# Performance work log

Hardware: AMD Instinct MI355X
Metric: run time of the kernel (lower is better)

## Reference

```python
import jax, jax.numpy as jnp
import numpy as np

T, B, H, I = 128, 32, 256, 256


def setup_inputs() -> dict:
    key = jax.random.key(0)
    ks = jax.random.split(key, 8)
    s = 0.05
    embs = jax.random.normal(ks[0], (T, B, I), jnp.float32)
    lens = jax.random.randint(ks[1], (B,), 1, T + 1)  # lengths in [1, T]
    W_ih = jax.random.normal(ks[2], (4 * H, I), jnp.float32) * s
    W_hh = jax.random.normal(ks[3], (4 * H, H), jnp.float32) * s
    b_ih = jax.random.normal(ks[4], (4 * H,), jnp.float32) * s
    b_hh = jax.random.normal(ks[5], (4 * H,), jnp.float32) * s
    W_a = jax.random.normal(ks[6], (H, 2 * H), jnp.float32) * s  # attention combine (Luong-style)
    b_a = jax.random.normal(ks[7], (H,), jnp.float32) * s
    return {"embs": embs, "lens": lens, "W_ih": W_ih, "W_hh": W_hh,
            "b_ih": b_ih, "b_hh": b_hh, "W_a": W_a, "b_a": b_a}


def reference(embs, lens, W_ih, W_hh, b_ih, b_hh, W_a, b_a):
    Tn, Bn, _ = embs.shape
    Hn = W_hh.shape[1]
    t_idx = jnp.arange(Tn)

    def step(carry, inp):
        h, c, buf, h_fin, c_fin = carry  # h,c: [B,H]; buf: [T,B,H] history of outputs
        t, emb = inp
        # dot-product attention of current hidden over past outputs (steps < t)
        scores = jnp.einsum('tbh,bh->tb', buf, h)
        valid = (t_idx < t)[:, None]
        alpha = jax.nn.softmax(jnp.where(valid, scores, -1e9), axis=0)
        ctx = jnp.einsum('tb,tbh->bh', alpha, buf)
        h_att = jnp.tanh(jnp.concatenate([ctx, h], axis=-1) @ W_a.T + b_a)
        h = jnp.where(t > 0, h_att, h)  # no history at t=0
        # standard PyTorch LSTM cell (gate order i,f,g,o)
        gates = emb @ W_ih.T + b_ih + h @ W_hh.T + b_hh
        i_g, f_g, g_g, o_g = jnp.split(gates, 4, axis=-1)
        c = jax.nn.sigmoid(f_g) * c + jax.nn.sigmoid(i_g) * jnp.tanh(g_g)
        h = jax.nn.sigmoid(o_g) * jnp.tanh(c)
        buf = buf.at[t].set(h)
        take = (t == lens - 1)[:, None]
        h_fin = jnp.where(take, h, h_fin)
        c_fin = jnp.where(take, c, c_fin)
        return (h, c, buf, h_fin, c_fin), h

    z = jnp.zeros((Bn, Hn), embs.dtype)
    buf0 = jnp.zeros((Tn, Bn, Hn), embs.dtype)
    carry, output = jax.lax.scan(step, (z, z, buf0, z, z), (t_idx, embs))
    # output: [T,B,H]; final (h,c) gathered at t == lens-1: [B,H]
    return output, carry[3], carry[4]
```

## Files before the change

### kernel.cpp

```cpp
#include <hip/hip_runtime.h>


#define T_DIM 128
#define B_DIM 32

typedef _Float16 half2_t __attribute__((ext_vector_type(2)));

static __device__ __forceinline__ unsigned pack2(float a, float b) {
  half2_t h;
  h.x = (_Float16)a;
  h.y = (_Float16)b;
  return __builtin_bit_cast(unsigned, h);
}

static __device__ __forceinline__ float dot2f(unsigned w, unsigned v, float acc) {
  half2_t a = __builtin_bit_cast(half2_t, w);
  half2_t b = __builtin_bit_cast(half2_t, v);
#if __has_builtin(__builtin_amdgcn_fdot2)
  return __builtin_amdgcn_fdot2(a, b, acc, false);
#else
  return acc + (float)a.x * (float)b.x + (float)a.y * (float)b.y;
#endif
}

static __device__ __forceinline__ float dot8(uint4 w, uint4 v, float acc) {
  acc = dot2f(w.x, v.x, acc);
  acc = dot2f(w.y, v.y, acc);
  acc = dot2f(w.z, v.z, acc);
  acc = dot2f(w.w, v.w, acc);
  return acc;
}

static __device__ __forceinline__ float lo16(unsigned u) {
  return (float)__builtin_bit_cast(half2_t, u).x;
}
static __device__ __forceinline__ float hi16(unsigned u) {
  return (float)__builtin_bit_cast(half2_t, u).y;
}

static __device__ __forceinline__ float fsig(float x) {
  return __builtin_amdgcn_rcpf(1.f + __expf(-x));
}
static __device__ __forceinline__ float ftanh(float x) {
  float e = __expf(2.f * x);
  return 1.f - 2.f * __builtin_amdgcn_rcpf(e + 1.f);
}

__global__ void pack_weights(const float* __restrict__ W_ih, const float* __restrict__ W_hh,
                             const float* __restrict__ W_a, float* __restrict__ W_ihT,
                             uint4* __restrict__ Whh_pack, uint4* __restrict__ Wa_pack,
                             unsigned long long* __restrict__ ywp,
                             unsigned long long* __restrict__ psx) {
  int n = blockIdx.x * 256 + threadIdx.x;
  {
    int k = n >> 10, r = n & 1023;
    W_ihT[n] = W_ih[r * 256 + k];
  }
  if (n < 32768) {
    int m = n >> 12, tid = (n >> 3) & 511, i = n & 7;
    int r_local = tid >> 2, qk = tid & 3;
    int q = r_local >> 5, jl = r_local & 31;
    int r = q * 256 + m * 32 + jl;
    const float* src = W_hh + r * 256 + (4 * i + qk) * 8;
    uint4 v;
    v.x = pack2(src[0], src[1]);
    v.y = pack2(src[2], src[3]);
    v.z = pack2(src[4], src[5]);
    v.w = pack2(src[6], src[7]);
    Whh_pack[n] = v;
  }
  if (n < 16384) {
    int m = n >> 11, j = (n >> 3) & 255, c = n & 7;
    int col0 = (c < 4) ? (m * 32 + c * 8) : (256 + m * 32 + (c - 4) * 8);
    const float* src = W_a + j * 512 + col0;
    uint4 v;
    v.x = pack2(src[0], src[1]);
    v.y = pack2(src[2], src[3]);
    v.z = pack2(src[4], src[5]);
    v.w = pack2(src[6], src[7]);
    Wa_pack[n] = v;
  }
  if (n < 65536)
    __hip_atomic_store(&ywp[n], 0ull, __ATOMIC_RELAXED, __HIP_MEMORY_SCOPE_AGENT);
  else if (n < 81920)
    __hip_atomic_store(&psx[n - 65536], 0ull, __ATOMIC_RELAXED, __HIP_MEMORY_SCOPE_AGENT);
}

__global__ void compute_gih(const float* __restrict__ embs, const float* __restrict__ W_ihT,
                            const float* __restrict__ b_ih, const float* __restrict__ b_hh,
                            float* __restrict__ gih) {
  __shared__ float embS[8][256];
  const int tid = threadIdx.x;
  const int tb0 = blockIdx.x * 8;
#pragma unroll
  for (int e = 0; e < 8; ++e) embS[e][tid] = embs[(size_t)(tb0 + e) * 256 + tid];
  __syncthreads();
  float acc[8][4];
#pragma unroll
  for (int e = 0; e < 8; ++e)
#pragma unroll
    for (int q = 0; q < 4; ++q) acc[e][q] = 0.f;
  for (int k = 0; k < 256; ++k) {
    float w0 = W_ihT[k * 1024 + tid];
    float w1 = W_ihT[k * 1024 + tid + 256];
    float w2 = W_ihT[k * 1024 + tid + 512];
    float w3 = W_ihT[k * 1024 + tid + 768];
#pragma unroll
    for (int e = 0; e < 8; ++e) {
      float x = embS[e][k];
      acc[e][0] += x * w0;
      acc[e][1] += x * w1;
      acc[e][2] += x * w2;
      acc[e][3] += x * w3;
    }
  }
#pragma unroll
  for (int q = 0; q < 4; ++q) {
    float bias = b_ih[q * 256 + tid] + b_hh[q * 256 + tid];
#pragma unroll
    for (int e = 0; e < 8; ++e)
      gih[(size_t)(tb0 + e) * 1024 + q * 256 + tid] = acc[e][q] + bias;
  }
}

__global__ void __launch_bounds__(512, 1)
alstm_rec(const int* __restrict__ lens, const float* __restrict__ gih,
          const uint4* __restrict__ Whh_pack, const uint4* __restrict__ Wa_pack,
          const float* __restrict__ b_a, unsigned long long* __restrict__ ywp,
          unsigned long long* __restrict__ psx, float* __restrict__ out,
          float* __restrict__ hfin, float* __restrict__ cfin) {
  const int tid = threadIdx.x;
  const int b = blockIdx.x & 31;
  const int m = blockIdx.x >> 5;

  __shared__ __align__(16) unsigned histSl[128 * 18];
  __shared__ __align__(16) float ystoreF[128 * 256];
  __shared__ __align__(16) unsigned hp2[128];
  __shared__ __align__(16) float sc[128];
  __shared__ __align__(16) float zp[8][256];
  __shared__ float gsl[128];

  uint4 wh4[8];
  {
    const uint4* p = Whh_pack + ((size_t)m * 512 + tid) * 8;
#pragma unroll
    for (int i = 0; i < 8; ++i) wh4[i] = p[i];
  }
  uint4 way[4], waw[4];
  {
    const int j_pub = (tid - 128) & 255;
    const uint4* p = Wa_pack + ((size_t)m * 256 + j_pub) * 8;
#pragma unroll
    for (int i = 0; i < 4; ++i) way[i] = p[i];
#pragma unroll
    for (int i = 0; i < 4; ++i) waw[i] = p[4 + i];
  }
  const float ba_j = (tid < 256) ? b_a[tid] : 0.f;
  const int len_b = lens[b];
  const int r_local = tid >> 2, qk = tid & 3;
  const int gq = r_local >> 5, gjl = r_local & 31;

  if (tid < 128) hp2[tid] = 0u;
  float c_reg = 0.f;
  __syncthreads();

  for (int t = 0; t < T_DIM; ++t) {
    float gih_v = gih[((size_t)t * 32 + b) * 1024 + gq * 256 + m * 32 + gjl];
    float w_j = 0.f;

    if (t > 0) {
      if (tid < 256) {
        const unsigned long long* base = ywp + b * 2048 + tid;
        unsigned long long v[8];
        for (;;) {
          bool ok = true;
#pragma unroll
          for (int mm = 0; mm < 8; ++mm)
            v[mm] = __hip_atomic_load(base + mm * 256, __ATOMIC_RELAXED, __HIP_MEMORY_SCOPE_AGENT);
#pragma unroll
          for (int mm = 0; mm < 8; ++mm) ok &= ((unsigned)v[mm] == (unsigned)t);
          if (ok) break;
          __builtin_amdgcn_s_sleep(1);
        }
        float y = 0.f, w = 0.f;
#pragma unroll
        for (int mm = 0; mm < 8; ++mm) {
          unsigned pl = (unsigned)(v[mm] >> 32);
          y += lo16(pl);
          w += hi16(pl);
        }
        w_j = w;
        ystoreF[(t - 1) * 256 + tid] = y;
      } else if (tid < 320) {
        const int p = tid - 256;
        const unsigned long long* base = psx + b * 512 + p;
        unsigned long long v[8];
        for (;;) {
          bool ok = true;
#pragma unroll
          for (int mm = 0; mm < 8; ++mm)
            v[mm] = __hip_atomic_load(base + mm * 64, __ATOMIC_RELAXED, __HIP_MEMORY_SCOPE_AGENT);
#pragma unroll
          for (int mm = 0; mm < 8; ++mm) ok &= ((unsigned)v[mm] == (unsigned)t);
          if (ok) break;
          __builtin_amdgcn_s_sleep(1);
        }
        float s0 = 0.f, s1 = 0.f;
#pragma unroll
        for (int mm = 0; mm < 8; ++mm) {
          unsigned pl = (unsigned)(v[mm] >> 32);
          s0 += lo16(pl);
          s1 += hi16(pl);
        }
        float v0 = (2 * p < t) ? s0 : -3.0e38f;
        float v1 = (2 * p + 1 < t) ? s1 : -3.0e38f;
        float mx = fmaxf(v0, v1);
#pragma unroll
        for (int off = 32; off >= 1; off >>= 1) mx = fmaxf(mx, __shfl_xor(mx, off));
        float e0 = (2 * p < t) ? __expf(v0 - mx) : 0.f;
        float e1 = (2 * p + 1 < t) ? __expf(v1 - mx) : 0.f;
        float sm = e0 + e1;
#pragma unroll
        for (int off = 32; off >= 1; off >>= 1) sm += __shfl_xor(sm, off);
        float inv = __builtin_amdgcn_rcpf(sm);
        sc[2 * p] = e0 * inv;
        sc[2 * p + 1] = e1 * inv;
      }
      __syncthreads();
      {
        const int sp = tid >> 6, cg = tid & 63;
        float c0 = 0.f, c1 = 0.f, c2 = 0.f, c3 = 0.f;
        const float* yb = ystoreF + 4 * cg;
        for (int s = sp; s < t; s += 8) {
          float al = sc[s];
          const float4 yv = *(const float4*)(yb + (size_t)s * 256);
          c0 += al * yv.x;
          c1 += al * yv.y;
          c2 += al * yv.z;
          c3 += al * yv.w;
        }
        float4 st;
        st.x = c0;
        st.y = c1;
        st.z = c2;
        st.w = c3;
        *(float4*)&zp[sp][4 * cg] = st;
      }
      __syncthreads();
      if (tid < 256) {
        float z = 0.f;
#pragma unroll
        for (int p = 0; p < 8; ++p) z += zp[p][tid];
        float hv = ftanh(ba_j + w_j + z);
        float o = __shfl_xor(hv, 1);
        if (!(tid & 1)) hp2[tid >> 1] = pack2(hv, o);
      }
      __syncthreads();
    }
    {
      float a0 = 0.f, a1 = 0.f;
#pragma unroll
      for (int i = 0; i < 8; i += 2) {
        uint4 hv0 = *(const uint4*)&hp2[(4 * i + qk) << 2];
        uint4 hv1 = *(const uint4*)&hp2[(4 * (i + 1) + qk) << 2];
        a0 = dot8(wh4[i], hv0, a0);
        a1 = dot8(wh4[i + 1], hv1, a1);
      }
      float a = a0 + a1;
      a += __shfl_xor(a, 1);
      a += __shfl_xor(a, 2);
      if (qk == 0) gsl[r_local] = a + gih_v;
    }
    __syncthreads();
    unsigned hq[16];
    {
      const int sl = tid & 31;
      float ig = fsig(gsl[sl]);
      float fg = fsig(gsl[32 + sl]);
      float gg = ftanh(gsl[64 + sl]);
      float og = fsig(gsl[96 + sl]);
      float cn = fg * c_reg + ig * gg;
      float hn = og * ftanh(cn);
      c_reg = cn;
      if (tid >= 384 && tid < 416) {
        out[((size_t)t * 32 + b) * 256 + m * 32 + sl] = hn;
        if (t == len_b - 1) {
          hfin[b * 256 + m * 32 + sl] = hn;
          cfin[b * 256 + m * 32 + sl] = cn;
        }
      }
      float o = __shfl_xor(hn, 1);
      unsigned u = pack2(hn, o);
      if (tid >= 384 && tid < 416 && !(tid & 1)) histSl[t * 18 + (sl >> 1)] = u;
#pragma unroll
      for (int k = 0; k < 16; ++k) hq[k] = __shfl(u, 2 * k);
    }
    if (tid < 128) {
      float a0 = 0.f, a1 = 0.f;
      if (tid == t) {
#pragma unroll
        for (int k = 0; k < 8; ++k) {
          a0 = dot2f(hq[2 * k], hq[2 * k], a0);
          a1 = dot2f(hq[2 * k + 1], hq[2 * k + 1], a1);
        }
      } else {
#pragma unroll
        for (int k = 0; k < 8; ++k) {
          uint2 hw = *(const uint2*)&histSl[tid * 18 + 2 * k];
          a0 = dot2f(hw.x, hq[2 * k], a0);
          a1 = dot2f(hw.y, hq[2 * k + 1], a1);
        }
      }
      float a = a0 + a1;
      float o = __shfl_xor(a, 1);
      if (!(tid & 1)) {
        unsigned long long vv = ((unsigned long long)pack2(a, o) << 32) |
                                (unsigned long long)(unsigned)(t + 1);
        __hip_atomic_store(&psx[b * 512 + m * 64 + (tid >> 1)], vv, __ATOMIC_RELAXED,
                           __HIP_MEMORY_SCOPE_AGENT);
      }
    } else if (tid < 384) {
      const int j = tid - 128;
      uint4 hv0 = make_uint4(hq[0], hq[1], hq[2], hq[3]);
      uint4 hv1 = make_uint4(hq[4], hq[5], hq[6], hq[7]);
      uint4 hv2 = make_uint4(hq[8], hq[9], hq[10], hq[11]);
      uint4 hv3 = make_uint4(hq[12], hq[13], hq[14], hq[15]);
      float ay0 = 0.f, ay1 = 0.f, aw0 = 0.f, aw1 = 0.f;
      ay0 = dot8(way[0], hv0, ay0);
      aw0 = dot8(waw[0], hv0, aw0);
      ay1 = dot8(way[1], hv1, ay1);
      aw1 = dot8(waw[1], hv1, aw1);
      ay0 = dot8(way[2], hv2, ay0);
      aw0 = dot8(waw[2], hv2, aw0);
      ay1 = dot8(way[3], hv3, ay1);
      aw1 = dot8(waw[3], hv3, aw1);
      unsigned long long vv = ((unsigned long long)pack2(ay0 + ay1, aw0 + aw1) << 32) |
                              (unsigned long long)(unsigned)(t + 1);
      __hip_atomic_store(&ywp[b * 2048 + m * 256 + j], vv, __ATOMIC_RELAXED,
                         __HIP_MEMORY_SCOPE_AGENT);
    }
  }
}

extern "C" void kernel_launch(void* const* d_in, const int* in_sizes, int n_in,
                              void* d_out, int out_size, void* d_ws, size_t ws_size,
                              hipStream_t stream) {
  const float* embs = (const float*)d_in[0];
  const int* lens = (const int*)d_in[1];
  const float* W_ih = (const float*)d_in[2];
  const float* W_hh = (const float*)d_in[3];
  const float* b_ih = (const float*)d_in[4];
  const float* b_hh = (const float*)d_in[5];
  const float* W_a = (const float*)d_in[6];
  const float* b_a = (const float*)d_in[7];

  float* out = (float*)d_out;
  float* hfin = out + (size_t)T_DIM * B_DIM * 256;
  float* cfin = hfin + (size_t)B_DIM * 256;

  char* ws = (char*)d_ws;
  float* gih = (float*)ws;
  float* W_ihT = (float*)(ws + 16777216);
  uint4* Whh_pack = (uint4*)(ws + 17825792);
  uint4* Wa_pack = (uint4*)(ws + 18350080);
  unsigned long long* ywp = (unsigned long long*)(ws + 18612224);
  unsigned long long* psx = (unsigned long long*)(ws + 19136512);

  pack_weights<<<1024, 256, 0, stream>>>(W_ih, W_hh, W_a, W_ihT, Whh_pack, Wa_pack, ywp, psx);
  compute_gih<<<512, 256, 0, stream>>>(embs, W_ihT, b_ih, b_hh, gih);
  alstm_rec<<<256, 512, 0, stream>>>(lens, gih, Whh_pack, Wa_pack, b_a, ywp, psx, out, hfin,
                                     cfin);
}
```

Measured before the change: 539.0 us.

## Split each batch row across 4 blocks instead of 8 in recurrent kernel

Each recurrent block now owns 64 hidden units instead of 32. This halves the grid to 128 blocks and halves the number of cross-block partial sums that must be polled and reduced each timestep. Weight packing, the flag buffers and the per-thread register arrays are widened to match (16 W_hh chunks, 8 W_a chunks, 32 h words per thread). The trade is fewer synchronising blocks against more serial work per block per step and higher register pressure. Changing the launch bound to 2 blocks per CU may also cap registers enough to cause spills.

```diff
diff --git a/kernel.cpp b/kernel.cpp
--- a/kernel.cpp
+++ b/kernel.cpp
@@ -57,11 +57,11 @@
     W_ihT[n] = W_ih[r * 256 + k];
   }
   if (n < 32768) {
-    int m = n >> 12, tid = (n >> 3) & 511, i = n & 7;
-    int r_local = tid >> 2, qk = tid & 3;
-    int q = r_local >> 5, jl = r_local & 31;
-    int r = q * 256 + m * 32 + jl;
-    const float* src = W_hh + r * 256 + (4 * i + qk) * 8;
+    int m = n >> 13, tid = (n >> 4) & 511, i = n & 15;
+    int r_local = tid >> 1, kh = tid & 1;
+    int q = r_local >> 6, jl = r_local & 63;
+    int r = q * 256 + m * 64 + jl;
+    const float* src = W_hh + r * 256 + kh * 128 + i * 8;
     uint4 v;
     v.x = pack2(src[0], src[1]);
     v.y = pack2(src[2], src[3]);
@@ -70,8 +70,8 @@
     Whh_pack[n] = v;
   }
   if (n < 16384) {
-    int m = n >> 11, j = (n >> 3) & 255, c = n & 7;
-    int col0 = (c < 4) ? (m * 32 + c * 8) : (256 + m * 32 + (c - 4) * 8);
+    int m = n >> 12, j = (n >> 4) & 255, c = n & 15;
+    int col0 = (c < 8) ? (m * 64 + c * 8) : (256 + m * 64 + (c - 8) * 8);
     const float* src = W_a + j * 512 + col0;
     uint4 v;
     v.x = pack2(src[0], src[1]);
@@ -80,10 +80,10 @@
     v.w = pack2(src[6], src[7]);
     Wa_pack[n] = v;
   }
-  if (n < 65536)
+  if (n < 32768)
     __hip_atomic_store(&ywp[n], 0ull, __ATOMIC_RELAXED, __HIP_MEMORY_SCOPE_AGENT);
-  else if (n < 81920)
-    __hip_atomic_store(&psx[n - 65536], 0ull, __ATOMIC_RELAXED, __HIP_MEMORY_SCOPE_AGENT);
+  else if (n < 40960)
+    __hip_atomic_store(&psx[n - 32768], 0ull, __ATOMIC_RELAXED, __HIP_MEMORY_SCOPE_AGENT);
 }
 
 __global__ void compute_gih(const float* __restrict__ embs, const float* __restrict__ W_ihT,
@@ -123,7 +123,7 @@
   }
 }
 
-__global__ void __launch_bounds__(512, 1)
+__global__ void __launch_bounds__(512, 2)
 alstm_rec(const int* __restrict__ lens, const float* __restrict__ gih,
           const uint4* __restrict__ Whh_pack, const uint4* __restrict__ Wa_pack,
           const float* __restrict__ b_a, unsigned long long* __restrict__ ywp,
@@ -133,58 +133,58 @@
   const int b = blockIdx.x & 31;
   const int m = blockIdx.x >> 5;
 
-  __shared__ __align__(16) unsigned histSl[128 * 18];
+  __shared__ __align__(16) unsigned histSl[128 * 34];
   __shared__ __align__(16) float ystoreF[128 * 256];
   __shared__ __align__(16) unsigned hp2[128];
   __shared__ __align__(16) float sc[128];
   __shared__ __align__(16) float zp[8][256];
-  __shared__ float gsl[128];
-
-  uint4 wh4[8];
+  __shared__ float gsl[256];
+
+  uint4 wh4[16];
   {
-    const uint4* p = Whh_pack + ((size_t)m * 512 + tid) * 8;
-#pragma unroll
-    for (int i = 0; i < 8; ++i) wh4[i] = p[i];
-  }
-  uint4 way[4], waw[4];
+    const uint4* p = Whh_pack + ((size_t)m * 512 + tid) * 16;
+#pragma unroll
+    for (int i = 0; i < 16; ++i) wh4[i] = p[i];
+  }
+  uint4 way[8], waw[8];
   {
     const int j_pub = (tid - 128) & 255;
-    const uint4* p = Wa_pack + ((size_t)m * 256 + j_pub) * 8;
-#pragma unroll
-    for (int i = 0; i < 4; ++i) way[i] = p[i];
-#pragma unroll
-    for (int i = 0; i < 4; ++i) waw[i] = p[4 + i];
+    const uint4* p = Wa_pack + ((size_t)m * 256 + j_pub) * 16;
+#pragma unroll
+    for (int i = 0; i < 8; ++i) way[i] = p[i];
+#pragma unroll
+    for (int i = 0; i < 8; ++i) waw[i] = p[8 + i];
   }
   const float ba_j = (tid < 256) ? b_a[tid] : 0.f;
   const int len_b = lens[b];
-  const int r_local = tid >> 2, qk = tid & 3;
-  const int gq = r_local >> 5, gjl = r_local & 31;
+  const int r_local = tid >> 1, kh = tid & 1;
+  const int gq = r_local >> 6, gjl = r_local & 63;
 
   if (tid < 128) hp2[tid] = 0u;
   float c_reg = 0.f;
   __syncthreads();
 
   for (int t = 0; t < T_DIM; ++t) {
-    float gih_v = gih[((size_t)t * 32 + b) * 1024 + gq * 256 + m * 32 + gjl];
+    float gih_v = gih[((size_t)t * 32 + b) * 1024 + gq * 256 + m * 64 + gjl];
     float w_j = 0.f;
 
     if (t > 0) {
       if (tid < 256) {
-        const unsigned long long* base = ywp + b * 2048 + tid;
-        unsigned long long v[8];
+        const unsigned long long* base = ywp + b * 1024 + tid;
+        unsigned long long v[4];
         for (;;) {
           bool ok = true;
 #pragma unroll
-          for (int mm = 0; mm < 8; ++mm)
+          for (int mm = 0; mm < 4; ++mm)
             v[mm] = __hip_atomic_load(base + mm * 256, __ATOMIC_RELAXED, __HIP_MEMORY_SCOPE_AGENT);
 #pragma unroll
-          for (int mm = 0; mm < 8; ++mm) ok &= ((unsigned)v[mm] == (unsigned)t);
+          for (int mm = 0; mm < 4; ++mm) ok &= ((unsigned)v[mm] == (unsigned)t);
           if (ok) break;
           __builtin_amdgcn_s_sleep(1);
         }
         float y = 0.f, w = 0.f;
 #pragma unroll
-        for (int mm = 0; mm < 8; ++mm) {
+        for (int mm = 0; mm < 4; ++mm) {
           unsigned pl = (unsigned)(v[mm] >> 32);
           y += lo16(pl);
           w += hi16(pl);
@@ -193,21 +193,21 @@
         ystoreF[(t - 1) * 256 + tid] = y;
       } else if (tid < 320) {
         const int p = tid - 256;
-        const unsigned long long* base = psx + b * 512 + p;
-        unsigned long long v[8];
+        const unsigned long long* base = psx + b * 256 + p;
+        unsigned long long v[4];
         for (;;) {
           bool ok = true;
 #pragma unroll
-          for (int mm = 0; mm < 8; ++mm)
+          for (int mm = 0; mm < 4; ++mm)
             v[mm] = __hip_atomic_load(base + mm * 64, __ATOMIC_RELAXED, __HIP_MEMORY_SCOPE_AGENT);
 #pragma unroll
-          for (int mm = 0; mm < 8; ++mm) ok &= ((unsigned)v[mm] == (unsigned)t);
+          for (int mm = 0; mm < 4; ++mm) ok &= ((unsigned)v[mm] == (unsigned)t);
           if (ok) break;
           __builtin_amdgcn_s_sleep(1);
         }
         float s0 = 0.f, s1 = 0.f;
 #pragma unroll
-        for (int mm = 0; mm < 8; ++mm) {
+        for (int mm = 0; mm < 4; ++mm) {
           unsigned pl = (unsigned)(v[mm] >> 32);
           s0 += lo16(pl);
           s1 += hi16(pl);
@@ -258,55 +258,59 @@
       __syncthreads();
     }
     {
-      float a0 = 0.f, a1 = 0.f;
-#pragma unroll
-      for (int i = 0; i < 8; i += 2) {
-        uint4 hv0 = *(const uint4*)&hp2[(4 * i + qk) << 2];
-        uint4 hv1 = *(const uint4*)&hp2[(4 * (i + 1) + qk) << 2];
-        a0 = dot8(wh4[i], hv0, a0);
-        a1 = dot8(wh4[i + 1], hv1, a1);
-      }
-      float a = a0 + a1;
+      const int pb = kh * 64;
+      float a0 = 0.f, a1 = 0.f, a2 = 0.f, a3 = 0.f;
+#pragma unroll
+      for (int i = 0; i < 16; i += 4) {
+        uint4 h0 = *(const uint4*)&hp2[pb + 4 * i];
+        uint4 h1 = *(const uint4*)&hp2[pb + 4 * (i + 1)];
+        uint4 h2 = *(const uint4*)&hp2[pb + 4 * (i + 2)];
+        uint4 h3 = *(const uint4*)&hp2[pb + 4 * (i + 3)];
+        a0 = dot8(wh4[i], h0, a0);
+        a1 = dot8(wh4[i + 1], h1, a1);
+        a2 = dot8(wh4[i + 2], h2, a2);
+        a3 = dot8(wh4[i + 3], h3, a3);
+      }
+      float a = (a0 + a1) + (a2 + a3);
       a += __shfl_xor(a, 1);
-      a += __shfl_xor(a, 2);
-      if (qk == 0) gsl[r_local] = a + gih_v;
+      if (kh == 0) gsl[r_local] = a + gih_v;
     }
     __syncthreads();
-    unsigned hq[16];
+    unsigned hq[32];
     {
-      const int sl = tid & 31;
+      const int sl = tid & 63;
       float ig = fsig(gsl[sl]);
-      float fg = fsig(gsl[32 + sl]);
-      float gg = ftanh(gsl[64 + sl]);
-      float og = fsig(gsl[96 + sl]);
+      float fg = fsig(gsl[64 + sl]);
+      float gg = ftanh(gsl[128 + sl]);
+      float og = fsig(gsl[192 + sl]);
       float cn = fg * c_reg + ig * gg;
       float hn = og * ftanh(cn);
       c_reg = cn;
-      if (tid >= 384 && tid < 416) {
-        out[((size_t)t * 32 + b) * 256 + m * 32 + sl] = hn;
+      if (tid >= 384 && tid < 448) {
+        out[((size_t)t * 32 + b) * 256 + m * 64 + sl] = hn;
         if (t == len_b - 1) {
-          hfin[b * 256 + m * 32 + sl] = hn;
-          cfin[b * 256 + m * 32 + sl] = cn;
+          hfin[b * 256 + m * 64 + sl] = hn;
+          cfin[b * 256 + m * 64 + sl] = cn;
         }
       }
       float o = __shfl_xor(hn, 1);
       unsigned u = pack2(hn, o);
-      if (tid >= 384 && tid < 416 && !(tid & 1)) histSl[t * 18 + (sl >> 1)] = u;
-#pragma unroll
-      for (int k = 0; k < 16; ++k) hq[k] = __shfl(u, 2 * k);
+      if (tid >= 384 && tid < 448 && !(tid & 1)) histSl[t * 34 + (sl >> 1)] = u;
+#pragma unroll
+      for (int k = 0; k < 32; ++k) hq[k] = __shfl(u, 2 * k);
     }
     if (tid < 128) {
       float a0 = 0.f, a1 = 0.f;
       if (tid == t) {
 #pragma unroll
-        for (int k = 0; k < 8; ++k) {
+        for (int k = 0; k < 16; ++k) {
           a0 = dot2f(hq[2 * k], hq[2 * k], a0);
           a1 = dot2f(hq[2 * k + 1], hq[2 * k + 1], a1);
         }
       } else {
 #pragma unroll
-        for (int k = 0; k < 8; ++k) {
-          uint2 hw = *(const uint2*)&histSl[tid * 18 + 2 * k];
+        for (int k = 0; k < 16; ++k) {
+          uint2 hw = *(const uint2*)&histSl[tid * 34 + 2 * k];
           a0 = dot2f(hw.x, hq[2 * k], a0);
           a1 = dot2f(hw.y, hq[2 * k + 1], a1);
         }
@@ -316,27 +320,24 @@
       if (!(tid & 1)) {
         unsigned long long vv = ((unsigned long long)pack2(a, o) << 32) |
                                 (unsigned long long)(unsigned)(t + 1);
-        __hip_atomic_store(&psx[b * 512 + m * 64 + (tid >> 1)], vv, __ATOMIC_RELAXED,
+        __hip_atomic_store(&psx[b * 256 + m * 64 + (tid >> 1)], vv, __ATOMIC_RELAXED,
                            __HIP_MEMORY_SCOPE_AGENT);
       }
     } else if (tid < 384) {
       const int j = tid - 128;
-      uint4 hv0 = make_uint4(hq[0], hq[1], hq[2], hq[3]);
-      uint4 hv1 = make_uint4(hq[4], hq[5], hq[6], hq[7]);
-      uint4 hv2 = make_uint4(hq[8], hq[9], hq[10], hq[11]);
-      uint4 hv3 = make_uint4(hq[12], hq[13], hq[14], hq[15]);
       float ay0 = 0.f, ay1 = 0.f, aw0 = 0.f, aw1 = 0.f;
-      ay0 = dot8(way[0], hv0, ay0);
-      aw0 = dot8(waw[0], hv0, aw0);
-      ay1 = dot8(way[1], hv1, ay1);
-      aw1 = dot8(waw[1], hv1, aw1);
-      ay0 = dot8(way[2], hv2, ay0);
-      aw0 = dot8(waw[2], hv2, aw0);
-      ay1 = dot8(way[3], hv3, ay1);
-      aw1 = dot8(waw[3], hv3, aw1);
+#pragma unroll
+      for (int c = 0; c < 8; c += 2) {
+        uint4 hv0 = make_uint4(hq[4 * c], hq[4 * c + 1], hq[4 * c + 2], hq[4 * c + 3]);
+        uint4 hv1 = make_uint4(hq[4 * c + 4], hq[4 * c + 5], hq[4 * c + 6], hq[4 * c + 7]);
+        ay0 = dot8(way[c], hv0, ay0);
+        aw0 = dot8(waw[c], hv0, aw0);
+        ay1 = dot8(way[c + 1], hv1, ay1);
+        aw1 = dot8(waw[c + 1], hv1, aw1);
+      }
       unsigned long long vv = ((unsigned long long)pack2(ay0 + ay1, aw0 + aw1) << 32) |
                               (unsigned long long)(unsigned)(t + 1);
-      __hip_atomic_store(&ywp[b * 2048 + m * 256 + j], vv, __ATOMIC_RELAXED,
+      __hip_atomic_store(&ywp[b * 1024 + m * 256 + j], vv, __ATOMIC_RELAXED,
                          __HIP_MEMORY_SCOPE_AGENT);
     }
   }
@@ -368,6 +369,6 @@
 
   pack_weights<<<1024, 256, 0, stream>>>(W_ih, W_hh, W_a, W_ihT, Whh_pack, Wa_pack, ywp, psx);
   compute_gih<<<512, 256, 0, stream>>>(embs, W_ihT, b_ih, b_hh, gih);
-  alstm_rec<<<256, 512, 0, stream>>>(lens, gih, Whh_pack, Wa_pack, b_a, ywp, psx, out, hfin,
+  alstm_rec<<<128, 512, 0, stream>>>(lens, gih, Whh_pack, Wa_pack, b_a, ywp, psx, out, hfin,
                                      cfin);
 }
```

Result: slower. 569.8 us (+5.7%).

## Exchange only packed hidden state across blocks; compute attention redundantly per block

Applied to the files above, without the earlier changes.

Each block now publishes just its 32-element slice of the new hidden state through a single flag-tagged word array, instead of publishing partial attention scores and partial W_a products for every block to sum. Every block reads the full hidden vector and recomputes scores, softmax, the W_a projection (weights held in 32 uint4 registers per thread) and the context sum locally from a full fp16 history kept in swizzled shared memory. This cuts the cross-block polling traffic and partial-sum reductions, at the cost of eight-fold redundant attention and projection arithmetic, extra __syncthreads, and much higher register and shared-memory use. Launch bounds also change to 2 blocks per SM.

```diff
diff --git a/kernel.cpp b/kernel.cpp
--- a/kernel.cpp
+++ b/kernel.cpp
@@ -48,9 +48,8 @@
 
 __global__ void pack_weights(const float* __restrict__ W_ih, const float* __restrict__ W_hh,
                              const float* __restrict__ W_a, float* __restrict__ W_ihT,
-                             uint4* __restrict__ Whh_pack, uint4* __restrict__ Wa_pack,
-                             unsigned long long* __restrict__ ywp,
-                             unsigned long long* __restrict__ psx) {
+                             uint4* __restrict__ Whh_pack, uint4* __restrict__ WaRow,
+                             unsigned long long* __restrict__ hx) {
   int n = blockIdx.x * 256 + threadIdx.x;
   {
     int k = n >> 10, r = n & 1023;
@@ -70,20 +69,17 @@
     Whh_pack[n] = v;
   }
   if (n < 16384) {
-    int m = n >> 11, j = (n >> 3) & 255, c = n & 7;
-    int col0 = (c < 4) ? (m * 32 + c * 8) : (256 + m * 32 + (c - 4) * 8);
-    const float* src = W_a + j * 512 + col0;
+    int type = n >> 13, j = (n >> 5) & 255, i = n & 31;
+    const float* src = W_a + j * 512 + type * 256 + i * 8;
     uint4 v;
     v.x = pack2(src[0], src[1]);
     v.y = pack2(src[2], src[3]);
     v.z = pack2(src[4], src[5]);
     v.w = pack2(src[6], src[7]);
-    Wa_pack[n] = v;
-  }
-  if (n < 65536)
-    __hip_atomic_store(&ywp[n], 0ull, __ATOMIC_RELAXED, __HIP_MEMORY_SCOPE_AGENT);
-  else if (n < 81920)
-    __hip_atomic_store(&psx[n - 65536], 0ull, __ATOMIC_RELAXED, __HIP_MEMORY_SCOPE_AGENT);
+    WaRow[n] = v;
+  }
+  if (n < 4096)
+    __hip_atomic_store(&hx[n], 0ull, __ATOMIC_RELAXED, __HIP_MEMORY_SCOPE_AGENT);
 }
 
 __global__ void compute_gih(const float* __restrict__ embs, const float* __restrict__ W_ihT,
@@ -123,21 +119,22 @@
   }
 }
 
-__global__ void __launch_bounds__(512, 1)
+__global__ void __launch_bounds__(512, 2)
 alstm_rec(const int* __restrict__ lens, const float* __restrict__ gih,
-          const uint4* __restrict__ Whh_pack, const uint4* __restrict__ Wa_pack,
-          const float* __restrict__ b_a, unsigned long long* __restrict__ ywp,
-          unsigned long long* __restrict__ psx, float* __restrict__ out,
-          float* __restrict__ hfin, float* __restrict__ cfin) {
+          const uint4* __restrict__ Whh_pack, const uint4* __restrict__ WaRow,
+          const float* __restrict__ b_a, unsigned long long* __restrict__ hx,
+          float* __restrict__ out, float* __restrict__ hfin, float* __restrict__ cfin) {
   const int tid = threadIdx.x;
   const int b = blockIdx.x & 31;
   const int m = blockIdx.x >> 5;
 
-  __shared__ __align__(16) unsigned histSl[128 * 18];
-  __shared__ __align__(16) float ystoreF[128 * 256];
-  __shared__ __align__(16) unsigned hp2[128];
+  __shared__ __align__(16) unsigned histF[128 * 128];
+  __shared__ __align__(16) unsigned ystore[128 * 128];
+  __shared__ __align__(16) unsigned hcur[128];
   __shared__ __align__(16) float sc[128];
   __shared__ __align__(16) float zp[8][256];
+  __shared__ __align__(16) float wsl[256];
+  __shared__ __align__(16) unsigned hp2[128];
   __shared__ float gsl[128];
 
   uint4 wh4[8];
@@ -146,14 +143,11 @@
 #pragma unroll
     for (int i = 0; i < 8; ++i) wh4[i] = p[i];
   }
-  uint4 way[4], waw[4];
+  uint4 wa[32];
   {
-    const int j_pub = (tid - 128) & 255;
-    const uint4* p = Wa_pack + ((size_t)m * 256 + j_pub) * 8;
-#pragma unroll
-    for (int i = 0; i < 4; ++i) way[i] = p[i];
-#pragma unroll
-    for (int i = 0; i < 4; ++i) waw[i] = p[4 + i];
+    const uint4* p = WaRow + ((size_t)(tid >> 8) * 256 + (tid & 255)) * 32;
+#pragma unroll
+    for (int i = 0; i < 32; ++i) wa[i] = p[i];
   }
   const float ba_j = (tid < 256) ? b_a[tid] : 0.f;
   const int len_b = lens[b];
@@ -166,78 +160,89 @@
 
   for (int t = 0; t < T_DIM; ++t) {
     float gih_v = gih[((size_t)t * 32 + b) * 1024 + gq * 256 + m * 32 + gjl];
-    float w_j = 0.f;
 
     if (t > 0) {
-      if (tid < 256) {
-        const unsigned long long* base = ywp + b * 2048 + tid;
-        unsigned long long v[8];
+      if (tid < 128) {
+        const unsigned long long* myhx = hx + b * 128 + tid;
+        unsigned long long v;
         for (;;) {
-          bool ok = true;
-#pragma unroll
-          for (int mm = 0; mm < 8; ++mm)
-            v[mm] = __hip_atomic_load(base + mm * 256, __ATOMIC_RELAXED, __HIP_MEMORY_SCOPE_AGENT);
-#pragma unroll
-          for (int mm = 0; mm < 8; ++mm) ok &= ((unsigned)v[mm] == (unsigned)t);
-          if (ok) break;
+          v = __hip_atomic_load(myhx, __ATOMIC_RELAXED, __HIP_MEMORY_SCOPE_AGENT);
+          if ((unsigned)v == (unsigned)t) break;
           __builtin_amdgcn_s_sleep(1);
         }
-        float y = 0.f, w = 0.f;
-#pragma unroll
-        for (int mm = 0; mm < 8; ++mm) {
-          unsigned pl = (unsigned)(v[mm] >> 32);
-          y += lo16(pl);
-          w += hi16(pl);
-        }
-        w_j = w;
-        ystoreF[(t - 1) * 256 + tid] = y;
-      } else if (tid < 320) {
+        unsigned pr = (unsigned)(v >> 32);
+        hcur[tid] = pr;
+        histF[(t - 1) * 128 + (tid ^ (((t - 1) & 7) << 2))] = pr;
+      }
+      __syncthreads();
+      if (r_local < t) {
+        const int sxz = (r_local & 7) << 2;
+        const int srow = r_local * 128;
+        const int cb = qk * 32;
+        float a0 = 0.f, a1 = 0.f;
+#pragma unroll
+        for (int k = 0; k < 8; k += 2) {
+          uint4 u0 = *(const uint4*)&histF[srow + ((cb + 4 * k) ^ sxz)];
+          uint4 u1 = *(const uint4*)&histF[srow + ((cb + 4 * (k + 1)) ^ sxz)];
+          uint4 q0 = *(const uint4*)&hcur[cb + 4 * k];
+          uint4 q1 = *(const uint4*)&hcur[cb + 4 * (k + 1)];
+          a0 = dot8(u0, q0, a0);
+          a1 = dot8(u1, q1, a1);
+        }
+        float a = a0 + a1;
+        a += __shfl_xor(a, 1);
+        a += __shfl_xor(a, 2);
+        if (qk == 0) sc[r_local] = a;
+      }
+      __syncthreads();
+      {
+        float a0 = 0.f, a1 = 0.f, a2 = 0.f, a3 = 0.f;
+#pragma unroll
+        for (int i = 0; i < 32; i += 4) {
+          uint4 h0 = *(const uint4*)&hcur[4 * i];
+          uint4 h1 = *(const uint4*)&hcur[4 * i + 4];
+          uint4 h2 = *(const uint4*)&hcur[4 * i + 8];
+          uint4 h3 = *(const uint4*)&hcur[4 * i + 12];
+          a0 = dot8(wa[i], h0, a0);
+          a1 = dot8(wa[i + 1], h1, a1);
+          a2 = dot8(wa[i + 2], h2, a2);
+          a3 = dot8(wa[i + 3], h3, a3);
+        }
+        float val = (a0 + a1) + (a2 + a3);
+        if (tid < 256) {
+          float o = __shfl_xor(val, 1);
+          if (!(tid & 1)) ystore[(t - 1) * 128 + (tid >> 1)] = pack2(val, o);
+        } else {
+          wsl[tid - 256] = val;
+        }
+      }
+      if (tid >= 256 && tid < 320) {
         const int p = tid - 256;
-        const unsigned long long* base = psx + b * 512 + p;
-        unsigned long long v[8];
-        for (;;) {
-          bool ok = true;
-#pragma unroll
-          for (int mm = 0; mm < 8; ++mm)
-            v[mm] = __hip_atomic_load(base + mm * 64, __ATOMIC_RELAXED, __HIP_MEMORY_SCOPE_AGENT);
-#pragma unroll
-          for (int mm = 0; mm < 8; ++mm) ok &= ((unsigned)v[mm] == (unsigned)t);
-          if (ok) break;
-          __builtin_amdgcn_s_sleep(1);
-        }
-        float s0 = 0.f, s1 = 0.f;
-#pragma unroll
-        for (int mm = 0; mm < 8; ++mm) {
-          unsigned pl = (unsigned)(v[mm] >> 32);
-          s0 += lo16(pl);
-          s1 += hi16(pl);
-        }
-        float v0 = (2 * p < t) ? s0 : -3.0e38f;
-        float v1 = (2 * p + 1 < t) ? s1 : -3.0e38f;
+        float v0 = (p < t) ? sc[p] : -3.0e38f;
+        float v1 = (p + 64 < t) ? sc[p + 64] : -3.0e38f;
         float mx = fmaxf(v0, v1);
 #pragma unroll
         for (int off = 32; off >= 1; off >>= 1) mx = fmaxf(mx, __shfl_xor(mx, off));
-        float e0 = (2 * p < t) ? __expf(v0 - mx) : 0.f;
-        float e1 = (2 * p + 1 < t) ? __expf(v1 - mx) : 0.f;
+        float e0 = (p < t) ? __expf(v0 - mx) : 0.f;
+        float e1 = (p + 64 < t) ? __expf(v1 - mx) : 0.f;
         float sm = e0 + e1;
 #pragma unroll
         for (int off = 32; off >= 1; off >>= 1) sm += __shfl_xor(sm, off);
         float inv = __builtin_amdgcn_rcpf(sm);
-        sc[2 * p] = e0 * inv;
-        sc[2 * p + 1] = e1 * inv;
+        sc[p] = e0 * inv;
+        sc[p + 64] = e1 * inv;
       }
       __syncthreads();
       {
         const int sp = tid >> 6, cg = tid & 63;
         float c0 = 0.f, c1 = 0.f, c2 = 0.f, c3 = 0.f;
-        const float* yb = ystoreF + 4 * cg;
         for (int s = sp; s < t; s += 8) {
           float al = sc[s];
-          const float4 yv = *(const float4*)(yb + (size_t)s * 256);
-          c0 += al * yv.x;
-          c1 += al * yv.y;
-          c2 += al * yv.z;
-          c3 += al * yv.w;
+          uint2 u = *(const uint2*)&ystore[s * 128 + 2 * cg];
+          c0 += al * lo16(u.x);
+          c1 += al * hi16(u.x);
+          c2 += al * lo16(u.y);
+          c3 += al * hi16(u.y);
         }
         float4 st;
         st.x = c0;
@@ -251,7 +256,7 @@
         float z = 0.f;
 #pragma unroll
         for (int p = 0; p < 8; ++p) z += zp[p][tid];
-        float hv = ftanh(ba_j + w_j + z);
+        float hv = ftanh(ba_j + wsl[tid] + z);
         float o = __shfl_xor(hv, 1);
         if (!(tid & 1)) hp2[tid >> 1] = pack2(hv, o);
       }
@@ -272,7 +277,6 @@
       if (qk == 0) gsl[r_local] = a + gih_v;
     }
     __syncthreads();
-    unsigned hq[16];
     {
       const int sl = tid & 31;
       float ig = fsig(gsl[sl]);
@@ -282,62 +286,21 @@
       float cn = fg * c_reg + ig * gg;
       float hn = og * ftanh(cn);
       c_reg = cn;
+      float o = __shfl_xor(hn, 1);
+      unsigned u = pack2(hn, o);
       if (tid >= 384 && tid < 416) {
         out[((size_t)t * 32 + b) * 256 + m * 32 + sl] = hn;
         if (t == len_b - 1) {
           hfin[b * 256 + m * 32 + sl] = hn;
           cfin[b * 256 + m * 32 + sl] = cn;
         }
-      }
-      float o = __shfl_xor(hn, 1);
-      unsigned u = pack2(hn, o);
-      if (tid >= 384 && tid < 416 && !(tid & 1)) histSl[t * 18 + (sl >> 1)] = u;
-#pragma unroll
-      for (int k = 0; k < 16; ++k) hq[k] = __shfl(u, 2 * k);
-    }
-    if (tid < 128) {
-      float a0 = 0.f, a1 = 0.f;
-      if (tid == t) {
-#pragma unroll
-        for (int k = 0; k < 8; ++k) {
-          a0 = dot2f(hq[2 * k], hq[2 * k], a0);
-          a1 = dot2f(hq[2 * k + 1], hq[2 * k + 1], a1);
-        }
-      } else {
-#pragma unroll
-        for (int k = 0; k < 8; ++k) {
-          uint2 hw = *(const uint2*)&histSl[tid * 18 + 2 * k];
-          a0 = dot2f(hw.x, hq[2 * k], a0);
-          a1 = dot2f(hw.y, hq[2 * k + 1], a1);
-        }
-      }
-      float a = a0 + a1;
-      float o = __shfl_xor(a, 1);
-      if (!(tid & 1)) {
-        unsigned long long vv = ((unsigned long long)pack2(a, o) << 32) |
-                                (unsigned long long)(unsigned)(t + 1);
-        __hip_atomic_store(&psx[b * 512 + m * 64 + (tid >> 1)], vv, __ATOMIC_RELAXED,
-                           __HIP_MEMORY_SCOPE_AGENT);
-      }
-    } else if (tid < 384) {
-      const int j = tid - 128;
-      uint4 hv0 = make_uint4(hq[0], hq[1], hq[2], hq[3]);
-      uint4 hv1 = make_uint4(hq[4], hq[5], hq[6], hq[7]);
-      uint4 hv2 = make_uint4(hq[8], hq[9], hq[10], hq[11]);
-      uint4 hv3 = make_uint4(hq[12], hq[13], hq[14], hq[15]);
-      float ay0 = 0.f, ay1 = 0.f, aw0 = 0.f, aw1 = 0.f;
-      ay0 = dot8(way[0], hv0, ay0);
-      aw0 = dot8(waw[0], hv0, aw0);
-      ay1 = dot8(way[1], hv1, ay1);
-      aw1 = dot8(waw[1], hv1, aw1);
-      ay0 = dot8(way[2], hv2, ay0);
-      aw0 = dot8(waw[2], hv2, aw0);
-      ay1 = dot8(way[3], hv3, ay1);
-      aw1 = dot8(waw[3], hv3, aw1);
-      unsigned long long vv = ((unsigned long long)pack2(ay0 + ay1, aw0 + aw1) << 32) |
-                              (unsigned long long)(unsigned)(t + 1);
-      __hip_atomic_store(&ywp[b * 2048 + m * 256 + j], vv, __ATOMIC_RELAXED,
-                         __HIP_MEMORY_SCOPE_AGENT);
+        if (!(tid & 1)) {
+          unsigned long long vv =
+              ((unsigned long long)u << 32) | (unsigned long long)(unsigned)(t + 1);
+          __hip_atomic_store(&hx[b * 128 + m * 16 + (sl >> 1)], vv, __ATOMIC_RELAXED,
+                             __HIP_MEMORY_SCOPE_AGENT);
+        }
+      }
     }
   }
 }
@@ -362,12 +325,10 @@
   float* gih = (float*)ws;
   float* W_ihT = (float*)(ws + 16777216);
   uint4* Whh_pack = (uint4*)(ws + 17825792);
-  uint4* Wa_pack = (uint4*)(ws + 18350080);
-  unsigned long long* ywp = (unsigned long long*)(ws + 18612224);
-  unsigned long long* psx = (unsigned long long*)(ws + 19136512);
-
-  pack_weights<<<1024, 256, 0, stream>>>(W_ih, W_hh, W_a, W_ihT, Whh_pack, Wa_pack, ywp, psx);
+  uint4* WaRow = (uint4*)(ws + 18350080);
+  unsigned long long* hx = (unsigned long long*)(ws + 18612224);
+
+  pack_weights<<<1024, 256, 0, stream>>>(W_ih, W_hh, W_a, W_ihT, Whh_pack, WaRow, hx);
   compute_gih<<<512, 256, 0, stream>>>(embs, W_ihT, b_ih, b_hh, gih);
-  alstm_rec<<<256, 512, 0, stream>>>(lens, gih, Whh_pack, Wa_pack, b_a, ywp, psx, out, hfin,
-                                     cfin);
-}
+  alstm_rec<<<256, 512, 0, stream>>>(lens, gih, Whh_pack, WaRow, b_a, hx, out, hfin, cfin);
+}
```

New measurement: 612.5 us. +13.6%, slower.
